# Optimization experiments

Hardware: AMD Instinct MI355X
Metric: run time of the kernel (lower is better)

The kernel has to match this reference:

```python
import jax, jax.numpy as jnp
import numpy as np

B = 4096        # batch (number of bags)
L = 64          # num_lookups per bag
NT = 4          # number of embedding tables
V = 500000      # rows per table
D = 128         # emb_dim
DENSE = 512     # dense feature dim
BOT = [512, 1024, 512, 128]
TOP = [D * (1 + NT), 1024, 512, 1]  # [640, 1024, 512, 1]


def _linear_params(key, dims):
    params = []
    for i in range(len(dims) - 1):
        din, dout = dims[i], dims[i + 1]
        kw, kb, key = jax.random.split(key, 3)
        sw = np.sqrt(2.0 / (din + dout)).astype(np.float32)
        sb = np.sqrt(1.0 / dout).astype(np.float32)
        params.append((sw * jax.random.normal(kw, (dout, din), jnp.float32),
                       sb * jax.random.normal(kb, (dout,), jnp.float32)))
    return params


def setup_inputs() -> dict:
    key = jax.random.key(0)
    k_dense, k_idx, k_tab, k_bot, k_top = jax.random.split(key, 5)
    inp = {}
    inp["x_dense"] = jax.random.normal(k_dense, (B, DENSE), jnp.float32)
    bound = float(np.sqrt(1.0 / V))
    inp["tables"] = jax.random.uniform(k_tab, (NT, V, D), jnp.float32, -bound, bound)
    bot = _linear_params(k_bot, BOT)
    top = _linear_params(k_top, TOP)
    inp["bw0"], inp["bb0"] = bot[0]
    inp["bw1"], inp["bb1"] = bot[1]
    inp["bw2"], inp["bb2"] = bot[2]
    inp["tw0"], inp["tb0"] = top[0]
    inp["tw1"], inp["tb1"] = top[1]
    inp["tw2"], inp["tb2"] = top[2]
    inp["x_indices"] = jax.random.randint(k_idx, (B * L, NT), 0, V, dtype=jnp.int32)
    inp["constant_offsets"] = jnp.arange(B, dtype=jnp.int32) * L  # offsets of each bag
    return inp


def reference(x_dense, tables, bw0, bb0, bw1, bb1, bw2, bb2,
              tw0, tb0, tw1, tb1, tw2, tb2, x_indices, constant_offsets):
    # bottom MLP: Linear+ReLU x3
    h = jax.nn.relu(x_dense @ bw0.T + bb0)
    h = jax.nn.relu(h @ bw1.T + bb1)
    bot_out = jax.nn.relu(h @ bw2.T + bb2)                     # [B, D]

    # EmbeddingBag (sum mode) per table, driven by offsets
    N = x_indices.shape[0]
    seg = jnp.searchsorted(constant_offsets, jnp.arange(N, dtype=constant_offsets.dtype),
                           side='right') - 1                    # [N] bag id per index
    gathered = jax.vmap(lambda tab, idx: tab[idx])(tables, x_indices.T)  # [NT, N, D]
    pooled = jax.vmap(lambda e: jax.ops.segment_sum(e, seg, num_segments=B))(gathered)  # [NT, B, D]

    # concat order: bottom MLP out, then tables 1..4 (columns 0..3)
    feat = jnp.concatenate([bot_out] + [pooled[t] for t in range(NT)], axis=1)  # [B, 640]

    # top MLP: ReLU, ReLU, Sigmoid
    z = jax.nn.relu(feat @ tw0.T + tb0)
    z = jax.nn.relu(z @ tw1.T + tb1)
    out = jax.nn.sigmoid(z @ tw2.T + tb2)                       # [B, 1]
    return out
```

## Files before the change

kernel.cpp:

```cpp
#include <hip/hip_runtime.h>
#include <hip/hip_bf16.h>
#include <cstdint>

#define B_BAGS 4096
#define L_LOOK 64
#define NT 4
#define V_ROWS 500000
#define D_EMB 128
#define FEAT 640

typedef _Float16 half8 __attribute__((ext_vector_type(8)));
typedef _Float16 half4 __attribute__((ext_vector_type(4)));
typedef float f32x4 __attribute__((ext_vector_type(4)));

#define GLOAD_LDS(g, l) __builtin_amdgcn_global_load_lds( \
    (const __attribute__((address_space(1))) void*)(g),   \
    (__attribute__((address_space(3))) void*)(l), 16, 0, 0)

template<int BM, int BN, bool RELU>
__device__ __forceinline__ void gemm_body(
    _Float16* lds, int bm, int bn,
    const _Float16* __restrict__ X, int ldx,
    const _Float16* __restrict__ W, int ldw,
    const float* __restrict__ bias,
    _Float16* __restrict__ Y, int ldy, int K)
{
    constexpr int BK = 64;
    constexpr int FM = BM / 32;
    constexpr int FN = BN / 32;
    constexpr int AI = BM * 8 / 256;
    constexpr int BI = BN * 8 / 256;

    _Float16* As = lds;
    _Float16* Bs = lds + BM * BK;

    const int tid  = threadIdx.x;
    const int lane = tid & 63;
    const int wave = tid >> 6;
    const int wm   = wave >> 1;
    const int wn   = wave & 1;
    const int q    = lane >> 4;
    const int r16  = lane & 15;

    f32x4 acc[FM][FN] = {};

    for (int k0 = 0; k0 < K; k0 += BK) {
#pragma unroll
        for (int i = 0; i < AI; ++i) {
            int L = i * 256 + tid;
            int row = L >> 3, sl = L & 7;
            const _Float16* src = X + (size_t)(bm + row) * ldx + k0 + ((sl ^ (row & 7)) * 8);
            GLOAD_LDS(src, As + (size_t)(i * 256 + wave * 64) * 8);
        }
#pragma unroll
        for (int j = 0; j < BI; ++j) {
            int L = j * 256 + tid;
            int row = L >> 3, sl = L & 7;
            const _Float16* src = W + (size_t)(bn + row) * ldw + k0 + ((sl ^ (row & 7)) * 8);
            GLOAD_LDS(src, Bs + (size_t)(j * 256 + wave * 64) * 8);
        }
        __syncthreads();

#pragma unroll
        for (int s = 0; s < 2; ++s) {
            half8 a[FM], b[FN];
#pragma unroll
            for (int i = 0; i < FM; ++i) {
                int R = wm * (BM / 2) + i * 16 + r16;
                int sl = (s * 4 + q) ^ (R & 7);
                a[i] = *(const half8*)(As + R * BK + sl * 8);
            }
#pragma unroll
            for (int j = 0; j < FN; ++j) {
                int R = wn * (BN / 2) + j * 16 + r16;
                int sl = (s * 4 + q) ^ (R & 7);
                b[j] = *(const half8*)(Bs + R * BK + sl * 8);
            }
#pragma unroll
            for (int i = 0; i < FM; ++i)
#pragma unroll
                for (int j = 0; j < FN; ++j)
                    acc[i][j] = __builtin_amdgcn_mfma_f32_16x16x32_f16(
                        a[i], b[j], acc[i][j], 0, 0, 0);
        }
        __syncthreads();
    }

#pragma unroll
    for (int i = 0; i < FM; ++i) {
        const int m0 = bm + wm * (BM / 2) + i * 16 + q * 4;
#pragma unroll
        for (int j = 0; j < FN; ++j) {
            const int n = bn + wn * (BN / 2) + j * 16 + r16;
            const float bv = bias[n];
#pragma unroll
            for (int e = 0; e < 4; ++e) {
                float o = acc[i][j][e] + bv;
                if (RELU) o = fmaxf(o, 0.f);
                Y[(size_t)(m0 + e) * ldy + n] = (_Float16)o;
            }
        }
    }
}

template<int BM, int BN, bool RELU>
__device__ __forceinline__ void gemm_body_f32(
    _Float16* lds, int bm, int bn,
    const float* __restrict__ X, int ldx,
    const float* __restrict__ W, int ldw,
    const float* __restrict__ bias,
    _Float16* __restrict__ Y, int ldy, int K)
{
    constexpr int BK = 64;
    constexpr int FM = BM / 32;
    constexpr int FN = BN / 32;
    constexpr int AI = BM * 8 / 256;
    constexpr int BI = BN * 8 / 256;

    _Float16* As = lds;
    _Float16* Bs = lds + BM * BK;

    const int tid  = threadIdx.x;
    const int lane = tid & 63;
    const int wave = tid >> 6;
    const int wm   = wave >> 1;
    const int wn   = wave & 1;
    const int q    = lane >> 4;
    const int r16  = lane & 15;

    f32x4 acc[FM][FN] = {};

    for (int k0 = 0; k0 < K; k0 += BK) {
#pragma unroll
        for (int i = 0; i < AI; ++i) {
            int S = i * 256 + tid;
            int row = S >> 3, c = S & 7;
            const float* src = X + (size_t)(bm + row) * ldx + k0 + c * 8;
            float4 v0 = *(const float4*)src;
            float4 v1 = *(const float4*)(src + 4);
            half8 h = { (_Float16)v0.x, (_Float16)v0.y, (_Float16)v0.z, (_Float16)v0.w,
                        (_Float16)v1.x, (_Float16)v1.y, (_Float16)v1.z, (_Float16)v1.w };
            *(half8*)(As + row * BK + ((c ^ (row & 7)) * 8)) = h;
        }
#pragma unroll
        for (int j = 0; j < BI; ++j) {
            int S = j * 256 + tid;
            int row = S >> 3, c = S & 7;
            const float* src = W + (size_t)(bn + row) * ldw + k0 + c * 8;
            float4 v0 = *(const float4*)src;
            float4 v1 = *(const float4*)(src + 4);
            half8 h = { (_Float16)v0.x, (_Float16)v0.y, (_Float16)v0.z, (_Float16)v0.w,
                        (_Float16)v1.x, (_Float16)v1.y, (_Float16)v1.z, (_Float16)v1.w };
            *(half8*)(Bs + row * BK + ((c ^ (row & 7)) * 8)) = h;
        }
        __syncthreads();

#pragma unroll
        for (int s = 0; s < 2; ++s) {
            half8 a[FM], b[FN];
#pragma unroll
            for (int i = 0; i < FM; ++i) {
                int R = wm * (BM / 2) + i * 16 + r16;
                int sl = (s * 4 + q) ^ (R & 7);
                a[i] = *(const half8*)(As + R * BK + sl * 8);
            }
#pragma unroll
            for (int j = 0; j < FN; ++j) {
                int R = wn * (BN / 2) + j * 16 + r16;
                int sl = (s * 4 + q) ^ (R & 7);
                b[j] = *(const half8*)(Bs + R * BK + sl * 8);
            }
#pragma unroll
            for (int i = 0; i < FM; ++i)
#pragma unroll
                for (int j = 0; j < FN; ++j)
                    acc[i][j] = __builtin_amdgcn_mfma_f32_16x16x32_f16(
                        a[i], b[j], acc[i][j], 0, 0, 0);
        }
        __syncthreads();
    }

#pragma unroll
    for (int i = 0; i < FM; ++i) {
        const int m0 = bm + wm * (BM / 2) + i * 16 + q * 4;
#pragma unroll
        for (int j = 0; j < FN; ++j) {
            const int n = bn + wn * (BN / 2) + j * 16 + r16;
            const float bv = bias[n];
#pragma unroll
            for (int e = 0; e < 4; ++e) {
                float o = acc[i][j][e] + bv;
                if (RELU) o = fmaxf(o, 0.f);
                Y[(size_t)(m0 + e) * ldy + n] = (_Float16)o;
            }
        }
    }
}

__device__ __forceinline__ void emb_body(
    int bag,
    const float* __restrict__ tables,
    const int*   __restrict__ idx,
    _Float16*    __restrict__ feat)
{
    const int wave = threadIdx.x >> 6;
    const int lane = threadIdx.x & 63;
    const int l5   = lane >> 5;
    const int c    = lane & 31;

    const int my_idx = idx[((size_t)bag * L_LOOK + lane) * NT + wave];
    const float* tab = tables + (size_t)wave * V_ROWS * D_EMB;

    float4 acc = {0.f, 0.f, 0.f, 0.f};
#pragma unroll 16
    for (int j = 0; j < 32; ++j) {
        int r = __shfl(my_idx, 2 * j + l5, 64);
        float4 v = ((const float4*)(tab + (size_t)r * D_EMB))[c];
        acc.x += v.x; acc.y += v.y; acc.z += v.z; acc.w += v.w;
    }
    acc.x += __shfl_xor(acc.x, 32, 64);
    acc.y += __shfl_xor(acc.y, 32, 64);
    acc.z += __shfl_xor(acc.z, 32, 64);
    acc.w += __shfl_xor(acc.w, 32, 64);
    if (l5 == 0) {
        half4 h = { (_Float16)acc.x, (_Float16)acc.y, (_Float16)acc.z, (_Float16)acc.w };
        *(half4*)(feat + (size_t)bag * FEAT + D_EMB + wave * D_EMB + c * 4) = h;
    }
}

struct GD {
    const _Float16* X; const _Float16* W; const float* bias; _Float16* Y;
    int ldx, ldw, ldy, K, m0, mTiles;
};

__global__ __launch_bounds__(256, 3) void mega(
    GD gA, int nA,
    int embBase, int embCount,
    const float* __restrict__ tables, const int* __restrict__ idx,
    _Float16* __restrict__ feat)
{
    __shared__ __align__(16) _Float16 lds[(128 + 128) * 64];
    int bid = blockIdx.x;
    if (bid < nA) {
        gemm_body<128, 128, true>(lds, gA.m0 + (bid % gA.mTiles) * 128,
                                  (bid / gA.mTiles) * 128,
                                  gA.X, gA.ldx, gA.W, gA.ldw, gA.bias,
                                  gA.Y, gA.ldy, gA.K);
        return;
    }
    bid -= nA;
    emb_body(embBase + bid, tables, idx, feat);
}

struct CvtRest {
    const float* src[5];
    _Float16*    dst[5];
    int          n4[5];
};

__global__ __launch_bounds__(256, 3) void fused1(
    const float* __restrict__ X, const float* __restrict__ W,
    const float* __restrict__ bias, _Float16* __restrict__ Y,
    CvtRest cvt,
    const float* __restrict__ tables, const int* __restrict__ idx,
    _Float16* __restrict__ feat)
{
    __shared__ __align__(16) _Float16 lds[(128 + 128) * 64];
    int bid = blockIdx.x;
    if (bid < 256) {
        gemm_body_f32<128, 128, true>(lds, (bid & 31) * 128, (bid >> 5) * 128,
                                      X, 512, W, 512, bias, Y, 1024, 512);
        return;
    }
    bid -= 256;
    if (bid < 64) {
        const int t0 = bid * 256 + threadIdx.x;
        const int stride = 64 * 256;
#pragma unroll
        for (int t = 0; t < 5; ++t) {
            const float4* s = (const float4*)cvt.src[t];
            half4* d = (half4*)cvt.dst[t];
            for (int i = t0; i < cvt.n4[t]; i += stride) {
                float4 v = s[i];
                half4 h = { (_Float16)v.x, (_Float16)v.y, (_Float16)v.z, (_Float16)v.w };
                d[i] = h;
            }
        }
        return;
    }
    emb_body(bid - 64, tables, idx, feat);
}

template<int BM, int BN, bool RELU>
__global__ __launch_bounds__(256, 3) void gemm_h(
    const _Float16* __restrict__ X, int ldx,
    const _Float16* __restrict__ W, int ldw,
    const float* __restrict__ bias,
    _Float16* __restrict__ Y, int ldy,
    int K)
{
    __shared__ __align__(16) _Float16 lds[(BM + BN) * 64];
    gemm_body<BM, BN, RELU>(lds, blockIdx.y * BM, blockIdx.x * BN,
                            X, ldx, W, ldw, bias, Y, ldy, K);
}

__global__ __launch_bounds__(256) void top2_h(
    const _Float16* __restrict__ Z,
    const _Float16* __restrict__ w,
    const float* __restrict__ bsc,
    float* __restrict__ out)
{
    const int row  = blockIdx.x * 4 + (threadIdx.x >> 6);
    const int lane = threadIdx.x & 63;

    half8 z  = *(const half8*)(Z + (size_t)row * 512 + lane * 8);
    half8 wv = *(const half8*)(w + lane * 8);
    float s = 0.f;
#pragma unroll
    for (int i = 0; i < 8; ++i) s += (float)z[i] * (float)wv[i];
#pragma unroll
    for (int off = 32; off > 0; off >>= 1) s += __shfl_down(s, off, 64);
    if (lane == 0) {
        float x = s + bsc[0];
        out[row] = 1.f / (1.f + expf(-x));
    }
}

extern "C" void kernel_launch(void* const* d_in, const int* in_sizes, int n_in,
                              void* d_out, int out_size, void* d_ws, size_t ws_size,
                              hipStream_t stream) {
    const float* x_dense = (const float*)d_in[0];
    const float* tables  = (const float*)d_in[1];
    const float* bw0 = (const float*)d_in[2];
    const float* bb0 = (const float*)d_in[3];
    const float* bw1 = (const float*)d_in[4];
    const float* bb1 = (const float*)d_in[5];
    const float* bw2 = (const float*)d_in[6];
    const float* bb2 = (const float*)d_in[7];
    const float* tw0 = (const float*)d_in[8];
    const float* tb0 = (const float*)d_in[9];
    const float* tw1 = (const float*)d_in[10];
    const float* tb1 = (const float*)d_in[11];
    const float* tw2 = (const float*)d_in[12];
    const float* tb2 = (const float*)d_in[13];
    const int*   x_idx = (const int*)d_in[14];
    float* out = (float*)d_out;

    char* p = (char*)d_ws;
    auto alloc = [&](size_t bytes) {
        char* r = p; p += (bytes + 255) & ~(size_t)255; return r;
    };
    _Float16* bw1h = (_Float16*)alloc((size_t)512 * 1024 * 2);
    _Float16* bw2h = (_Float16*)alloc((size_t)128 * 512 * 2);
    _Float16* tw0h = (_Float16*)alloc((size_t)1024 * 640 * 2);
    _Float16* tw1h = (_Float16*)alloc((size_t)512 * 1024 * 2);
    _Float16* tw2h = (_Float16*)alloc((size_t)512 * 2);
    _Float16* h0h  = (_Float16*)alloc((size_t)4096 * 1024 * 2);
    _Float16* h1h  = (_Float16*)alloc((size_t)4096 * 512 * 2);
    _Float16* feat = (_Float16*)alloc((size_t)4096 * 640 * 2);
    _Float16* z0h  = (_Float16*)alloc((size_t)4096 * 1024 * 2);
    _Float16* z1h  = (_Float16*)alloc((size_t)4096 * 512 * 2);

    CvtRest cr;
    cr.src[0] = bw1; cr.dst[0] = bw1h; cr.n4[0] = 512 * 1024 / 4;
    cr.src[1] = bw2; cr.dst[1] = bw2h; cr.n4[1] = 128 * 512 / 4;
    cr.src[2] = tw0; cr.dst[2] = tw0h; cr.n4[2] = 1024 * 640 / 4;
    cr.src[3] = tw1; cr.dst[3] = tw1h; cr.n4[3] = 512 * 1024 / 4;
    cr.src[4] = tw2; cr.dst[4] = tw2h; cr.n4[4] = 512 / 4;

    dim3 blk(256);

    GD g2;
    g2.X = h0h; g2.W = bw1h; g2.bias = bb1; g2.Y = h1h;
    g2.ldx = 1024; g2.ldw = 1024; g2.ldy = 512; g2.K = 1024; g2.m0 = 0; g2.mTiles = 32;

    GD g3;
    g3.X = h1h; g3.W = bw2h; g3.bias = bb2; g3.Y = feat;
    g3.ldx = 512; g3.ldw = 512; g3.ldy = 640; g3.K = 512; g3.m0 = 0; g3.mTiles = 32;

    fused1<<<dim3(256 + 64 + 2048), blk, 0, stream>>>(
        x_dense, bw0, bb0, h0h, cr, tables, x_idx, feat);

    mega<<<dim3(128 + 1280), blk, 0, stream>>>(
        g2, 128, 2048, 1280, tables, x_idx, feat);

    mega<<<dim3(32 + 768), blk, 0, stream>>>(
        g3, 32, 3328, 768, tables, x_idx, feat);

    gemm_h<64, 128, true><<<dim3(8, 64), blk, 0, stream>>>(
        feat, 640, tw0h, 640, tb0, z0h, 1024, 640);

    gemm_h<64, 128, true><<<dim3(4, 64), blk, 0, stream>>>(
        z0h, 1024, tw1h, 1024, tb1, z1h, 512, 1024);

    top2_h<<<dim3(1024), blk, 0, stream>>>(z1h, tw2h, tb2, out);
}
```

Baseline: 161.5 us.

## Fuse second top-MLP GEMM with final dot-product and sigmoid via atomics

Replaces the separate 1024→512 GEMM and the final 512→1 dot/sigmoid kernel with one kernel. Its epilogue applies bias and ReLU, multiplies by the last-layer weights and reduces partial sums across lanes. It then atomically accumulates per-row results into a global buffer, and the last contributor, found via a per-row counter, applies the sigmoid. This removes the z1 intermediate write and read and one kernel launch. In exchange it adds a memset of the accumulator and counters, global atomics, and a floating-point summation order that is no longer fixed.

```diff
diff --git a/kernel.cpp b/kernel.cpp
--- a/kernel.cpp
+++ b/kernel.cpp
@@ -304,25 +304,130 @@
                             X, ldx, W, ldw, bias, Y, ldy, K);
 }
 
-__global__ __launch_bounds__(256) void top2_h(
-    const _Float16* __restrict__ Z,
-    const _Float16* __restrict__ w,
-    const float* __restrict__ bsc,
+__global__ __launch_bounds__(256, 3) void top1_fused(
+    const _Float16* __restrict__ X,
+    const _Float16* __restrict__ W,
+    const float* __restrict__ bias,
+    const _Float16* __restrict__ w2,
+    const float* __restrict__ tb2,
+    float* __restrict__ accb,
+    unsigned int* __restrict__ ctrb,
     float* __restrict__ out)
 {
-    const int row  = blockIdx.x * 4 + (threadIdx.x >> 6);
-    const int lane = threadIdx.x & 63;
-
-    half8 z  = *(const half8*)(Z + (size_t)row * 512 + lane * 8);
-    half8 wv = *(const half8*)(w + lane * 8);
-    float s = 0.f;
-#pragma unroll
-    for (int i = 0; i < 8; ++i) s += (float)z[i] * (float)wv[i];
-#pragma unroll
-    for (int off = 32; off > 0; off >>= 1) s += __shfl_down(s, off, 64);
-    if (lane == 0) {
-        float x = s + bsc[0];
-        out[row] = 1.f / (1.f + expf(-x));
+    constexpr int BM = 64, BN = 128, BK = 64;
+    constexpr int FM = BM / 32;
+    constexpr int FN = BN / 32;
+    constexpr int AI = BM * 8 / 256;
+    constexpr int BI = BN * 8 / 256;
+    const int K = 1024;
+
+    __shared__ __align__(16) _Float16 lds[(BM + BN) * BK];
+    _Float16* As = lds;
+    _Float16* Bs = lds + BM * BK;
+
+    const int bm = blockIdx.y * BM;
+    const int bn = blockIdx.x * BN;
+    const int tid  = threadIdx.x;
+    const int lane = tid & 63;
+    const int wave = tid >> 6;
+    const int wm   = wave >> 1;
+    const int wn   = wave & 1;
+    const int q    = lane >> 4;
+    const int r16  = lane & 15;
+
+    f32x4 acc[FM][FN] = {};
+
+    for (int k0 = 0; k0 < K; k0 += BK) {
+#pragma unroll
+        for (int i = 0; i < AI; ++i) {
+            int L = i * 256 + tid;
+            int row = L >> 3, sl = L & 7;
+            const _Float16* src = X + (size_t)(bm + row) * 1024 + k0 + ((sl ^ (row & 7)) * 8);
+            GLOAD_LDS(src, As + (size_t)(i * 256 + wave * 64) * 8);
+        }
+#pragma unroll
+        for (int j = 0; j < BI; ++j) {
+            int L = j * 256 + tid;
+            int row = L >> 3, sl = L & 7;
+            const _Float16* src = W + (size_t)(bn + row) * 1024 + k0 + ((sl ^ (row & 7)) * 8);
+            GLOAD_LDS(src, Bs + (size_t)(j * 256 + wave * 64) * 8);
+        }
+        __syncthreads();
+
+#pragma unroll
+        for (int s = 0; s < 2; ++s) {
+            half8 a[FM], b[FN];
+#pragma unroll
+            for (int i = 0; i < FM; ++i) {
+                int R = wm * (BM / 2) + i * 16 + r16;
+                int sl = (s * 4 + q) ^ (R & 7);
+                a[i] = *(const half8*)(As + R * BK + sl * 8);
+            }
+#pragma unroll
+            for (int j = 0; j < FN; ++j) {
+                int R = wn * (BN / 2) + j * 16 + r16;
+                int sl = (s * 4 + q) ^ (R & 7);
+                b[j] = *(const half8*)(Bs + R * BK + sl * 8);
+            }
+#pragma unroll
+            for (int i = 0; i < FM; ++i)
+#pragma unroll
+                for (int j = 0; j < FN; ++j)
+                    acc[i][j] = __builtin_amdgcn_mfma_f32_16x16x32_f16(
+                        a[i], b[j], acc[i][j], 0, 0, 0);
+        }
+        __syncthreads();
+    }
+
+    float part[FM][4];
+#pragma unroll
+    for (int i = 0; i < FM; ++i)
+#pragma unroll
+        for (int e = 0; e < 4; ++e) part[i][e] = 0.f;
+
+#pragma unroll
+    for (int j = 0; j < FN; ++j) {
+        const int n = bn + wn * (BN / 2) + j * 16 + r16;
+        const float bv = bias[n];
+        const float wv = (float)w2[n];
+#pragma unroll
+        for (int i = 0; i < FM; ++i)
+#pragma unroll
+            for (int e = 0; e < 4; ++e) {
+                float v = fmaxf(acc[i][j][e] + bv, 0.f);
+                part[i][e] += v * wv;
+            }
+    }
+#pragma unroll
+    for (int mask = 1; mask < 16; mask <<= 1) {
+#pragma unroll
+        for (int i = 0; i < FM; ++i)
+#pragma unroll
+            for (int e = 0; e < 4; ++e)
+                part[i][e] += __shfl_xor(part[i][e], mask, 64);
+    }
+
+    if (r16 == 0) {
+#pragma unroll
+        for (int i = 0; i < FM; ++i)
+#pragma unroll
+            for (int e = 0; e < 4; ++e) {
+                int m = bm + wm * (BM / 2) + i * 16 + q * 4 + e;
+                atomicAdd(&accb[m], part[i][e]);
+            }
+        __threadfence();
+#pragma unroll
+        for (int i = 0; i < FM; ++i)
+#pragma unroll
+            for (int e = 0; e < 4; ++e) {
+                int m = bm + wm * (BM / 2) + i * 16 + q * 4 + e;
+                unsigned int c = atomicAdd(&ctrb[m], 1u);
+                if (c == 7u) {
+                    float tot = atomicAdd(&accb[m], 0.0f);
+                    float x = tot + tb2[0];
+                    out[m] = 1.f / (1.f + expf(-x));
+                }
+            }
     }
 }
 
@@ -359,7 +464,8 @@
     _Float16* h1h  = (_Float16*)alloc((size_t)4096 * 512 * 2);
     _Float16* feat = (_Float16*)alloc((size_t)4096 * 640 * 2);
     _Float16* z0h  = (_Float16*)alloc((size_t)4096 * 1024 * 2);
-    _Float16* z1h  = (_Float16*)alloc((size_t)4096 * 512 * 2);
+    float*        accb = (float*)alloc((size_t)4096 * 4);
+    unsigned int* ctrb = (unsigned int*)alloc((size_t)4096 * 4);
 
     CvtRest cr;
     cr.src[0] = bw1; cr.dst[0] = bw1h; cr.n4[0] = 512 * 1024 / 4;
@@ -378,6 +484,8 @@
     g3.X = h1h; g3.W = bw2h; g3.bias = bb2; g3.Y = feat;
     g3.ldx = 512; g3.ldw = 512; g3.ldy = 640; g3.K = 512; g3.m0 = 0; g3.mTiles = 32;
 
+    hipMemsetAsync(accb, 0, (size_t)4096 * 4 * 2, stream);
+
     fused1<<<dim3(256 + 64 + 2048), blk, 0, stream>>>(
         x_dense, bw0, bb0, h0h, cr, tables, x_idx, feat);
 
@@ -390,8 +498,6 @@
     gemm_h<64, 128, true><<<dim3(8, 64), blk, 0, stream>>>(
         feat, 640, tw0h, 640, tb0, z0h, 1024, 640);
 
-    gemm_h<64, 128, true><<<dim3(4, 64), blk, 0, stream>>>(
-        z0h, 1024, tw1h, 1024, tb1, z1h, 512, 1024);
-
-    top2_h<<<dim3(1024), blk, 0, stream>>>(z1h, tw2h, tb2, out);
-}
+    top1_fused<<<dim3(4, 64), blk, 0, stream>>>(
+        z0h, tw1h, tb1, tw2h, tb2, accb, ctrb, out);
+}
```

Result: slower. 181.5 us (+12.4%).
